# Optimization experiments

Measured on AMD Instinct MI355X. Metric: run time of the kernel, lower is better.

## Reference

```python
import jax, jax.numpy as jnp
import numpy as np

N_LAYERS = 3
NUM_USERS = 100000
NUM_ITEMS = 50000
N_NODES = NUM_USERS + NUM_ITEMS
N_EDGES = 6000000
EMB = 64


def setup_inputs() -> dict:
    key = jax.random.key(0)
    k1, k2, k3, k4, k5, k6, k7 = jax.random.split(key, 7)
    user_indices = jax.random.randint(k1, (1024,), 0, NUM_USERS)
    item_indices = jax.random.randint(k2, (1024,), 0, NUM_ITEMS)
    adj_src = jax.random.randint(k3, (N_EDGES,), 0, N_NODES)
    adj_dst = jax.random.randint(k4, (N_EDGES,), 0, N_NODES)
    # normalized adjacency values (stand-in for D^-1/2 A D^-1/2 entries)
    adj_vals = jax.random.uniform(k5, (N_EDGES,), dtype=jnp.float32) * 0.05
    user_emb = jax.random.normal(k6, (NUM_USERS, EMB), dtype=jnp.float32) * 0.1
    item_emb = jax.random.normal(k7, (NUM_ITEMS, EMB), dtype=jnp.float32) * 0.1
    return {
        "user_indices": user_indices,
        "item_indices": item_indices,
        "adj_src": adj_src,
        "adj_dst": adj_dst,
        "adj_vals": adj_vals,
        "user_emb": user_emb,
        "item_emb": item_emb,
    }


def reference(user_indices, item_indices, adj_src, adj_dst, adj_vals, user_emb, item_emb):
    # LightGCN.computer(): all_emb = cat(users, items); repeated SpMM; mean over layers
    all_emb = jnp.concatenate([user_emb, item_emb], axis=0)  # [N, d]
    n = all_emb.shape[0]
    cur = all_emb
    acc = all_emb  # running sum over layer embeddings (fused, avoids stacking)
    for _ in range(N_LAYERS):
        # SpMM in COO form: out[dst] += val * cur[src]
        msgs = adj_vals[:, None] * cur[adj_src]  # [E, d]
        cur = jax.ops.segment_sum(msgs, adj_dst, num_segments=n)
        acc = acc + cur
    light_out = acc / jnp.float32(N_LAYERS + 1)  # mean over (n_layers+1) embeddings
    # forward() returns cat(all_users, all_items) == light_out
    return light_out
```

## Files before the change

kernel.cpp:

```cpp
#include <hip/hip_runtime.h>


#define NUM_USERS 100000
#define NUM_ITEMS 50000
#define N_NODES   150000
#define EMB       64
#define N_EDGES   6000000

#define ROWS_PER_B 256
#define NBUCKETS   586
#define NROWS_PAD  (NBUCKETS * ROWS_PER_B)
#define PART_BLOCKS 256
#define CHUNK ((N_EDGES + PART_BLOCKS - 1) / PART_BLOCKS)

constexpr int NODE_F4 = N_NODES * EMB / 4;
constexpr int USER_F4 = NUM_USERS * EMB / 4;

typedef float f4v __attribute__((ext_vector_type(4)));

__device__ __forceinline__ float bf2f(unsigned short u) {
    union { unsigned int i; float f; } x; x.i = ((unsigned int)u) << 16; return x.f;
}
__device__ __forceinline__ unsigned short f2bf(float f) {
    union { float f; unsigned int i; } x; x.f = f;
    unsigned int b = x.i;
    return (unsigned short)((b + 0x7FFFu + ((b >> 16) & 1u)) >> 16);
}


__global__ void k_zero(int* __restrict__ p, int n) {
    int i = blockIdx.x * blockDim.x + threadIdx.x;
    if (i < n) p[i] = 0;
}

__global__ __launch_bounds__(256) void k_bhist(const int* __restrict__ dst,
                                               int* __restrict__ gcnt) {
    __shared__ int cnt[NBUCKETS];
    int t = threadIdx.x;
    for (int i = t; i < NBUCKETS; i += 256) cnt[i] = 0;
    __syncthreads();
    int e0 = blockIdx.x * CHUNK;
    int e1 = min(e0 + CHUNK, N_EDGES);
    int e = e0 + t;
    for (; e + 256 < e1; e += 512) {
        int b0 = __builtin_nontemporal_load(dst + e) >> 8;
        int b1 = __builtin_nontemporal_load(dst + e + 256) >> 8;
        atomicAdd(&cnt[b0], 1);
        atomicAdd(&cnt[b1], 1);
    }
    if (e < e1) atomicAdd(&cnt[__builtin_nontemporal_load(dst + e) >> 8], 1);
    __syncthreads();
    for (int i = t; i < NBUCKETS; i += 256)
        if (cnt[i]) atomicAdd(&gcnt[i], cnt[i]);
}

__global__ void k_bscan(const int* __restrict__ gcnt, int* __restrict__ boff,
                        int* __restrict__ gcur) {
    __shared__ int s[1024];
    int t = threadIdx.x;
    int x = (t < NBUCKETS) ? gcnt[t] : 0;
    s[t] = x;
    __syncthreads();
    for (int off = 1; off < 1024; off <<= 1) {
        int v = (t >= off) ? s[t - off] : 0;
        __syncthreads();
        s[t] += v;
        __syncthreads();
    }
    if (t < NBUCKETS) { int ex = s[t] - x; boff[t] = ex; gcur[t] = ex; }
    if (t == 0) boff[NBUCKETS] = N_EDGES;
}


__global__ __launch_bounds__(256) void k_part(const int* __restrict__ src,
                                              const int* __restrict__ dst,
                                              const float* __restrict__ val,
                                              int* __restrict__ gcur,
                                              int2* __restrict__ pairs) {
    __shared__ int cnt[NBUCKETS];
    __shared__ int base[NBUCKETS];
    int t = threadIdx.x;
    for (int i = t; i < NBUCKETS; i += 256) cnt[i] = 0;
    __syncthreads();
    int e0 = blockIdx.x * CHUNK;
    int e1 = min(e0 + CHUNK, N_EDGES);
    {
        int e = e0 + t;
        for (; e + 256 < e1; e += 512) {
            int b0 = __builtin_nontemporal_load(dst + e) >> 8;
            int b1 = __builtin_nontemporal_load(dst + e + 256) >> 8;
            atomicAdd(&cnt[b0], 1);
            atomicAdd(&cnt[b1], 1);
        }
        if (e < e1) atomicAdd(&cnt[__builtin_nontemporal_load(dst + e) >> 8], 1);
    }
    __syncthreads();
    for (int i = t; i < NBUCKETS; i += 256) {
        int c = cnt[i];
        base[i] = c ? atomicAdd(&gcur[i], c) : 0;
        cnt[i] = 0;
    }
    __syncthreads();
    {
        int e = e0 + t;
        for (; e + 256 < e1; e += 512) {
            int d0 = __builtin_nontemporal_load(dst + e);
            int s0 = __builtin_nontemporal_load(src + e);
            float v0 = __builtin_nontemporal_load(val + e);
            int d1 = __builtin_nontemporal_load(dst + e + 256);
            int s1 = __builtin_nontemporal_load(src + e + 256);
            float v1 = __builtin_nontemporal_load(val + e + 256);
            int b0 = d0 >> 8, b1 = d1 >> 8;
            int o0 = atomicAdd(&cnt[b0], 1);
            int o1 = atomicAdd(&cnt[b1], 1);
            pairs[base[b0] + o0] = make_int2(s0 | ((d0 & 255) << 18), __float_as_int(v0));
            pairs[base[b1] + o1] = make_int2(s1 | ((d1 & 255) << 18), __float_as_int(v1));
        }
        if (e < e1) {
            int d0 = __builtin_nontemporal_load(dst + e);
            int s0 = __builtin_nontemporal_load(src + e);
            float v0 = __builtin_nontemporal_load(val + e);
            int o0 = atomicAdd(&cnt[d0 >> 8], 1);
            pairs[base[d0 >> 8] + o0] = make_int2(s0 | ((d0 & 255) << 18),
                                                  __float_as_int(v0));
        }
    }
}


__global__ __launch_bounds__(256) void k_sort(const int* __restrict__ boff,
                                              const int2* __restrict__ pairs1,
                                              int2* __restrict__ pairs2,
                                              int* __restrict__ row_ptr) {
    __shared__ int cnt[ROWS_PER_B];
    __shared__ int s[ROWS_PER_B];
    int b = blockIdx.x;
    int t = threadIdx.x;
    cnt[t] = 0;
    __syncthreads();
    int beg = boff[b], end = boff[b + 1];
    {
        int e = beg + t;
        for (; e + 256 < end; e += 512) {
            int r0 = ((unsigned)pairs1[e].x) >> 18;
            int r1 = ((unsigned)pairs1[e + 256].x) >> 18;
            atomicAdd(&cnt[r0], 1);
            atomicAdd(&cnt[r1], 1);
        }
        if (e < end) atomicAdd(&cnt[((unsigned)pairs1[e].x) >> 18], 1);
    }
    __syncthreads();
    int x = cnt[t];
    s[t] = x;
    __syncthreads();
    for (int off = 1; off < 256; off <<= 1) {
        int v = (t >= off) ? s[t - off] : 0;
        __syncthreads();
        s[t] += v;
        __syncthreads();
    }
    int ex = beg + s[t] - x;
    row_ptr[b * ROWS_PER_B + t] = ex;
    if (b == NBUCKETS - 1 && t == 255) row_ptr[NROWS_PAD] = N_EDGES;
    __syncthreads();
    cnt[t] = ex;
    __syncthreads();
    const long* p1l = (const long*)pairs1;
    {
        int e = beg + t;
        for (; e + 256 < end; e += 512) {
            long q0 = __builtin_nontemporal_load(p1l + e);
            long q1 = __builtin_nontemporal_load(p1l + e + 256);
            int x0 = (int)q0, y0 = (int)(q0 >> 32);
            int x1 = (int)q1, y1 = (int)(q1 >> 32);
            int pos0 = atomicAdd(&cnt[((unsigned)x0) >> 18], 1);
            int pos1 = atomicAdd(&cnt[((unsigned)x1) >> 18], 1);
            pairs2[pos0] = make_int2(x0 & 0x3FFFF, y0);
            pairs2[pos1] = make_int2(x1 & 0x3FFFF, y1);
        }
        if (e < end) {
            long q0 = __builtin_nontemporal_load(p1l + e);
            int x0 = (int)q0, y0 = (int)(q0 >> 32);
            int pos0 = atomicAdd(&cnt[((unsigned)x0) >> 18], 1);
            pairs2[pos0] = make_int2(x0 & 0x3FFFF, y0);
        }
    }
}


__global__ void k_init(const f4v* __restrict__ ue, const f4v* __restrict__ ie,
                       ushort4* __restrict__ e0b, f4v* __restrict__ acc) {
    int i = blockIdx.x * blockDim.x + threadIdx.x;
    if (i >= NODE_F4) return;
    f4v v = (i < USER_F4) ? __builtin_nontemporal_load(ue + i)
                          : __builtin_nontemporal_load(ie + i - USER_F4);
    __builtin_nontemporal_store(v, acc + i);
    e0b[i] = make_ushort4(f2bf(v.x), f2bf(v.y), f2bf(v.z), f2bf(v.w));
}

__global__ __launch_bounds__(256) void k_spmm(const int* __restrict__ row_ptr,
                                              const long* __restrict__ pairs,
                                              const ushort4* __restrict__ cur,
                                              ushort4* __restrict__ nxt) {
    int tid = blockIdx.x * blockDim.x + threadIdx.x;
    int row = tid >> 4;
    if (row >= N_NODES) return;
    int c = tid & 15;
    int beg = row_ptr[row];
    int end = row_ptr[row + 1];
    float4 r = make_float4(0.f, 0.f, 0.f, 0.f);
    int k = beg;
    for (; k + 7 < end; k += 8) {
        long p[8];
        ushort4 g[8];
#pragma unroll
        for (int j = 0; j < 8; ++j) p[j] = pairs[k + j];
#pragma unroll
        for (int j = 0; j < 8; ++j) g[j] = cur[(long)(int)(p[j] & 0x3FFFF) * 16 + c];
#pragma unroll
        for (int j = 0; j < 8; ++j) {
            float v = __int_as_float((int)(p[j] >> 32));
            r.x += v * bf2f(g[j].x);
            r.y += v * bf2f(g[j].y);
            r.z += v * bf2f(g[j].z);
            r.w += v * bf2f(g[j].w);
        }
    }
    for (; k < end; ++k) {
        long p0 = pairs[k];
        ushort4 g0 = cur[(long)(int)(p0 & 0x3FFFF) * 16 + c];
        float v0 = __int_as_float((int)(p0 >> 32));
        r.x += v0 * bf2f(g0.x);
        r.y += v0 * bf2f(g0.y);
        r.z += v0 * bf2f(g0.z);
        r.w += v0 * bf2f(g0.w);
    }
    nxt[(long)row * 16 + c] = make_ushort4(f2bf(r.x), f2bf(r.y), f2bf(r.z), f2bf(r.w));
}

__global__ __launch_bounds__(256) void k_spmm_fin(const int* __restrict__ row_ptr,
                                                  const long* __restrict__ pairs,
                                                  const ushort4* __restrict__ cur,
                                                  const ushort4* __restrict__ e1b,
                                                  float4* __restrict__ acc) {
    int tid = blockIdx.x * blockDim.x + threadIdx.x;
    int row = tid >> 4;
    if (row >= N_NODES) return;
    int c = tid & 15;
    int beg = row_ptr[row];
    int end = row_ptr[row + 1];
    float4 r = make_float4(0.f, 0.f, 0.f, 0.f);
    int k = beg;
    for (; k + 7 < end; k += 8) {
        long p[8];
        ushort4 g[8];
#pragma unroll
        for (int j = 0; j < 8; ++j) p[j] = pairs[k + j];
#pragma unroll
        for (int j = 0; j < 8; ++j) g[j] = cur[(long)(int)(p[j] & 0x3FFFF) * 16 + c];
#pragma unroll
        for (int j = 0; j < 8; ++j) {
            float v = __int_as_float((int)(p[j] >> 32));
            r.x += v * bf2f(g[j].x);
            r.y += v * bf2f(g[j].y);
            r.z += v * bf2f(g[j].z);
            r.w += v * bf2f(g[j].w);
        }
    }
    for (; k < end; ++k) {
        long p0 = pairs[k];
        ushort4 g0 = cur[(long)(int)(p0 & 0x3FFFF) * 16 + c];
        float v0 = __int_as_float((int)(p0 >> 32));
        r.x += v0 * bf2f(g0.x);
        r.y += v0 * bf2f(g0.y);
        r.z += v0 * bf2f(g0.z);
        r.w += v0 * bf2f(g0.w);
    }
    long o = (long)row * 16 + c;
    ushort4 e1 = e1b[o];
    ushort4 e2 = cur[o];
    float4 a = acc[o];
    a.x = (a.x + bf2f(e1.x) + bf2f(e2.x) + r.x) * 0.25f;
    a.y = (a.y + bf2f(e1.y) + bf2f(e2.y) + r.y) * 0.25f;
    a.z = (a.z + bf2f(e1.z) + bf2f(e2.z) + r.z) * 0.25f;
    a.w = (a.w + bf2f(e1.w) + bf2f(e2.w) + r.w) * 0.25f;
    acc[o] = a;
}


__global__ void lgcn_init(const float4* __restrict__ user_emb,
                          const float4* __restrict__ item_emb,
                          float4* __restrict__ cur, float4* __restrict__ nxt,
                          float4* __restrict__ acc) {
    int i = blockIdx.x * blockDim.x + threadIdx.x;
    if (i >= NODE_F4) return;
    float4 v = (i < USER_F4) ? user_emb[i] : item_emb[i - USER_F4];
    cur[i] = v; acc[i] = v; nxt[i] = make_float4(0.f, 0.f, 0.f, 0.f);
}

__global__ void lgcn_scatter(const int* __restrict__ src, const int* __restrict__ dst,
                             const float* __restrict__ val,
                             const float4* __restrict__ cur, float* __restrict__ nxt) {
    int tid = blockIdx.x * blockDim.x + threadIdx.x;
    int e = tid >> 4;
    if (e >= N_EDGES) return;
    int c = tid & 15;
    int s = src[e]; int d = dst[e]; float v = val[e];
    float4 m = cur[(long)s * 16 + c];
    float* p = nxt + (long)d * 64 + c * 4;
    unsafeAtomicAdd(p + 0, v * m.x);
    unsafeAtomicAdd(p + 1, v * m.y);
    unsafeAtomicAdd(p + 2, v * m.z);
    unsafeAtomicAdd(p + 3, v * m.w);
}

__global__ void lgcn_add_zero(float4* __restrict__ acc, const float4* __restrict__ nxt,
                              float4* __restrict__ other) {
    int i = blockIdx.x * blockDim.x + threadIdx.x;
    if (i >= NODE_F4) return;
    float4 a = acc[i]; float4 n = nxt[i];
    a.x += n.x; a.y += n.y; a.z += n.z; a.w += n.w;
    acc[i] = a;
    other[i] = make_float4(0.f, 0.f, 0.f, 0.f);
}

__global__ void lgcn_final(float4* __restrict__ acc, const float4* __restrict__ nxt) {
    int i = blockIdx.x * blockDim.x + threadIdx.x;
    if (i >= NODE_F4) return;
    float4 a = acc[i]; float4 n = nxt[i];
    a.x = (a.x + n.x) * 0.25f; a.y = (a.y + n.y) * 0.25f;
    a.z = (a.z + n.z) * 0.25f; a.w = (a.w + n.w) * 0.25f;
    acc[i] = a;
}


extern "C" void kernel_launch(void* const* d_in, const int* in_sizes, int n_in,
                              void* d_out, int out_size, void* d_ws, size_t ws_size,
                              hipStream_t stream) {
    const int*    adj_src  = (const int*)d_in[2];
    const int*    adj_dst  = (const int*)d_in[3];
    const float*  adj_vals = (const float*)d_in[4];
    float* acc = (float*)d_out;

    const int BLK = 256;
    const int grid_node  = (NODE_F4 + BLK - 1) / BLK;
    const int grid_row16 = (N_NODES * 16 + BLK - 1) / BLK;

    const size_t SZ_PAIRS = (size_t)N_EDGES * 8;
    const size_t SZ_BF    = (size_t)N_NODES * EMB * 2;
    const size_t SZ_RP    = 600320;
    const size_t SZ_B     = 4096;
    const size_t NEEDED   = 2 * SZ_PAIRS + SZ_BF + SZ_RP + 3 * SZ_B;

    if (ws_size >= NEEDED) {
        char* w = (char*)d_ws;
        int2*    pairs2 = (int2*)(w);
        int2*    pairs1 = (int2*)(w + SZ_PAIRS);
        ushort4* e0b    = (ushort4*)(w + SZ_PAIRS);
        ushort4* e1b    = (ushort4*)(w + SZ_PAIRS + SZ_BF);
        ushort4* e2b    = (ushort4*)(w + 2 * SZ_PAIRS);
        int*  row_ptr= (int*)(w + 2 * SZ_PAIRS + SZ_BF);
        int*  gcnt   = (int*)(w + 2 * SZ_PAIRS + SZ_BF + SZ_RP);
        int*  boff   = (int*)(w + 2 * SZ_PAIRS + SZ_BF + SZ_RP + SZ_B);
        int*  gcur   = (int*)(w + 2 * SZ_PAIRS + SZ_BF + SZ_RP + 2 * SZ_B);

        k_zero<<<(NBUCKETS + BLK - 1) / BLK, BLK, 0, stream>>>(gcnt, NBUCKETS);
        k_bhist<<<PART_BLOCKS, BLK, 0, stream>>>(adj_dst, gcnt);
        k_bscan<<<1, 1024, 0, stream>>>(gcnt, boff, gcur);

        k_part<<<PART_BLOCKS, BLK, 0, stream>>>(adj_src, adj_dst, adj_vals, gcur, pairs1);

        k_sort<<<NBUCKETS, BLK, 0, stream>>>(boff, pairs1, pairs2, row_ptr);

        k_init<<<grid_node, BLK, 0, stream>>>((const f4v*)d_in[5], (const f4v*)d_in[6],
                                              e0b, (f4v*)acc);
        k_spmm<<<grid_row16, BLK, 0, stream>>>(row_ptr, (const long*)pairs2, e0b, e1b);
        k_spmm<<<grid_row16, BLK, 0, stream>>>(row_ptr, (const long*)pairs2, e1b, e2b);
        k_spmm_fin<<<grid_row16, BLK, 0, stream>>>(row_ptr, (const long*)pairs2, e2b,
                                                   e1b, (float4*)acc);
    } else {
        const float4* user_emb = (const float4*)d_in[5];
        const float4* item_emb = (const float4*)d_in[6];
        float* ws0 = (float*)d_ws;
        float* ws1 = ws0 + (size_t)N_NODES * EMB;
        lgcn_init<<<grid_node, BLK, 0, stream>>>(user_emb, item_emb,
                                                 (float4*)ws0, (float4*)ws1, (float4*)acc);
        lgcn_scatter<<<(N_EDGES*16+BLK-1)/BLK, BLK, 0, stream>>>(adj_src, adj_dst, adj_vals,
                                                    (const float4*)ws0, ws1);
        lgcn_add_zero<<<grid_node, BLK, 0, stream>>>((float4*)acc, (const float4*)ws1, (float4*)ws0);
        lgcn_scatter<<<(N_EDGES*16+BLK-1)/BLK, BLK, 0, stream>>>(adj_src, adj_dst, adj_vals,
                                                    (const float4*)ws1, ws0);
        lgcn_add_zero<<<grid_node, BLK, 0, stream>>>((float4*)acc, (const float4*)ws0, (float4*)ws1);
        lgcn_scatter<<<(N_EDGES*16+BLK-1)/BLK, BLK, 0, stream>>>(adj_src, adj_dst, adj_vals,
                                                    (const float4*)ws0, ws1);
        lgcn_final<<<grid_node, BLK, 0, stream>>>((float4*)acc, (const float4*)ws1);
    }
}
```

Baseline: 663.7 us.

## Replace two-pass bucket partition sort with direct per-row histogram and atomic placement

The CSR build no longer partitions edges into 256-row buckets and then sorts within each bucket. It now builds a per-destination-row histogram with global atomics, scans it hierarchically, and scatters each edge straight to its final slot through per-row atomic cursors. This drops one full pass over the pairs array and the intermediate buffer. In exchange it relies on heavy global atomic traffic and uncoalesced 8-byte scatters, and edge order within a row becomes nondeterministic.

```diff
diff --git a/kernel.cpp b/kernel.cpp
--- a/kernel.cpp
+++ b/kernel.cpp
@@ -10,8 +10,9 @@
 #define ROWS_PER_B 256
 #define NBUCKETS   586
 #define NROWS_PAD  (NBUCKETS * ROWS_PER_B)
-#define PART_BLOCKS 256
-#define CHUNK ((N_EDGES + PART_BLOCKS - 1) / PART_BLOCKS)
+
+#define HIST_BLOCKS  2048
+#define PLACE_BLOCKS 2048
 
 constexpr int NODE_F4 = N_NODES * EMB / 4;
 constexpr int USER_F4 = NUM_USERS * EMB / 4;
@@ -33,29 +34,28 @@
     if (i < n) p[i] = 0;
 }
 
-__global__ __launch_bounds__(256) void k_bhist(const int* __restrict__ dst,
-                                               int* __restrict__ gcnt) {
-    __shared__ int cnt[NBUCKETS];
-    int t = threadIdx.x;
-    for (int i = t; i < NBUCKETS; i += 256) cnt[i] = 0;
+__global__ __launch_bounds__(256) void k_rhist(const int* __restrict__ dst,
+                                               int* __restrict__ rcnt) {
+    int e = blockIdx.x * 256 + threadIdx.x;
+    int stride = gridDim.x * 256;
+    for (; e < N_EDGES; e += stride)
+        atomicAdd(&rcnt[dst[e]], 1);
+}
+
+__global__ __launch_bounds__(256) void k_bsum(const int* __restrict__ rcnt,
+                                              int* __restrict__ gcnt) {
+    __shared__ int s[256];
+    int b = blockIdx.x, t = threadIdx.x;
+    s[t] = rcnt[b * 256 + t];
     __syncthreads();
-    int e0 = blockIdx.x * CHUNK;
-    int e1 = min(e0 + CHUNK, N_EDGES);
-    int e = e0 + t;
-    for (; e + 256 < e1; e += 512) {
-        int b0 = __builtin_nontemporal_load(dst + e) >> 8;
-        int b1 = __builtin_nontemporal_load(dst + e + 256) >> 8;
-        atomicAdd(&cnt[b0], 1);
-        atomicAdd(&cnt[b1], 1);
-    }
-    if (e < e1) atomicAdd(&cnt[__builtin_nontemporal_load(dst + e) >> 8], 1);
-    __syncthreads();
-    for (int i = t; i < NBUCKETS; i += 256)
-        if (cnt[i]) atomicAdd(&gcnt[i], cnt[i]);
-}
-
-__global__ void k_bscan(const int* __restrict__ gcnt, int* __restrict__ boff,
-                        int* __restrict__ gcur) {
+    for (int off = 128; off > 0; off >>= 1) {
+        if (t < off) s[t] += s[t + off];
+        __syncthreads();
+    }
+    if (t == 0) gcnt[b] = s[0];
+}
+
+__global__ void k_bscan(const int* __restrict__ gcnt, int* __restrict__ boff) {
     __shared__ int s[1024];
     int t = threadIdx.x;
     int x = (t < NBUCKETS) ? gcnt[t] : 0;
@@ -67,90 +67,17 @@
         s[t] += v;
         __syncthreads();
     }
-    if (t < NBUCKETS) { int ex = s[t] - x; boff[t] = ex; gcur[t] = ex; }
+    if (t < NBUCKETS) boff[t] = s[t] - x;
     if (t == 0) boff[NBUCKETS] = N_EDGES;
 }
 
-
-__global__ __launch_bounds__(256) void k_part(const int* __restrict__ src,
-                                              const int* __restrict__ dst,
-                                              const float* __restrict__ val,
-                                              int* __restrict__ gcur,
-                                              int2* __restrict__ pairs) {
-    __shared__ int cnt[NBUCKETS];
-    __shared__ int base[NBUCKETS];
-    int t = threadIdx.x;
-    for (int i = t; i < NBUCKETS; i += 256) cnt[i] = 0;
-    __syncthreads();
-    int e0 = blockIdx.x * CHUNK;
-    int e1 = min(e0 + CHUNK, N_EDGES);
-    {
-        int e = e0 + t;
-        for (; e + 256 < e1; e += 512) {
-            int b0 = __builtin_nontemporal_load(dst + e) >> 8;
-            int b1 = __builtin_nontemporal_load(dst + e + 256) >> 8;
-            atomicAdd(&cnt[b0], 1);
-            atomicAdd(&cnt[b1], 1);
-        }
-        if (e < e1) atomicAdd(&cnt[__builtin_nontemporal_load(dst + e) >> 8], 1);
-    }
-    __syncthreads();
-    for (int i = t; i < NBUCKETS; i += 256) {
-        int c = cnt[i];
-        base[i] = c ? atomicAdd(&gcur[i], c) : 0;
-        cnt[i] = 0;
-    }
-    __syncthreads();
-    {
-        int e = e0 + t;
-        for (; e + 256 < e1; e += 512) {
-            int d0 = __builtin_nontemporal_load(dst + e);
-            int s0 = __builtin_nontemporal_load(src + e);
-            float v0 = __builtin_nontemporal_load(val + e);
-            int d1 = __builtin_nontemporal_load(dst + e + 256);
-            int s1 = __builtin_nontemporal_load(src + e + 256);
-            float v1 = __builtin_nontemporal_load(val + e + 256);
-            int b0 = d0 >> 8, b1 = d1 >> 8;
-            int o0 = atomicAdd(&cnt[b0], 1);
-            int o1 = atomicAdd(&cnt[b1], 1);
-            pairs[base[b0] + o0] = make_int2(s0 | ((d0 & 255) << 18), __float_as_int(v0));
-            pairs[base[b1] + o1] = make_int2(s1 | ((d1 & 255) << 18), __float_as_int(v1));
-        }
-        if (e < e1) {
-            int d0 = __builtin_nontemporal_load(dst + e);
-            int s0 = __builtin_nontemporal_load(src + e);
-            float v0 = __builtin_nontemporal_load(val + e);
-            int o0 = atomicAdd(&cnt[d0 >> 8], 1);
-            pairs[base[d0 >> 8] + o0] = make_int2(s0 | ((d0 & 255) << 18),
-                                                  __float_as_int(v0));
-        }
-    }
-}
-
-
-__global__ __launch_bounds__(256) void k_sort(const int* __restrict__ boff,
-                                              const int2* __restrict__ pairs1,
-                                              int2* __restrict__ pairs2,
-                                              int* __restrict__ row_ptr) {
-    __shared__ int cnt[ROWS_PER_B];
-    __shared__ int s[ROWS_PER_B];
-    int b = blockIdx.x;
-    int t = threadIdx.x;
-    cnt[t] = 0;
-    __syncthreads();
-    int beg = boff[b], end = boff[b + 1];
-    {
-        int e = beg + t;
-        for (; e + 256 < end; e += 512) {
-            int r0 = ((unsigned)pairs1[e].x) >> 18;
-            int r1 = ((unsigned)pairs1[e + 256].x) >> 18;
-            atomicAdd(&cnt[r0], 1);
-            atomicAdd(&cnt[r1], 1);
-        }
-        if (e < end) atomicAdd(&cnt[((unsigned)pairs1[e].x) >> 18], 1);
-    }
-    __syncthreads();
-    int x = cnt[t];
+__global__ __launch_bounds__(256) void k_rscan(const int* __restrict__ rcnt,
+                                               const int* __restrict__ boff,
+                                               int* __restrict__ row_ptr,
+                                               int* __restrict__ gcur) {
+    __shared__ int s[256];
+    int b = blockIdx.x, t = threadIdx.x;
+    int x = rcnt[b * 256 + t];
     s[t] = x;
     __syncthreads();
     for (int off = 1; off < 256; off <<= 1) {
@@ -159,31 +86,26 @@
         s[t] += v;
         __syncthreads();
     }
-    int ex = beg + s[t] - x;
-    row_ptr[b * ROWS_PER_B + t] = ex;
+    int ex = boff[b] + s[t] - x;
+    row_ptr[b * 256 + t] = ex;
+    gcur[b * 256 + t] = ex;
     if (b == NBUCKETS - 1 && t == 255) row_ptr[NROWS_PAD] = N_EDGES;
-    __syncthreads();
-    cnt[t] = ex;
-    __syncthreads();
-    const long* p1l = (const long*)pairs1;
-    {
-        int e = beg + t;
-        for (; e + 256 < end; e += 512) {
-            long q0 = __builtin_nontemporal_load(p1l + e);
-            long q1 = __builtin_nontemporal_load(p1l + e + 256);
-            int x0 = (int)q0, y0 = (int)(q0 >> 32);
-            int x1 = (int)q1, y1 = (int)(q1 >> 32);
-            int pos0 = atomicAdd(&cnt[((unsigned)x0) >> 18], 1);
-            int pos1 = atomicAdd(&cnt[((unsigned)x1) >> 18], 1);
-            pairs2[pos0] = make_int2(x0 & 0x3FFFF, y0);
-            pairs2[pos1] = make_int2(x1 & 0x3FFFF, y1);
-        }
-        if (e < end) {
-            long q0 = __builtin_nontemporal_load(p1l + e);
-            int x0 = (int)q0, y0 = (int)(q0 >> 32);
-            int pos0 = atomicAdd(&cnt[((unsigned)x0) >> 18], 1);
-            pairs2[pos0] = make_int2(x0 & 0x3FFFF, y0);
-        }
+}
+
+
+__global__ __launch_bounds__(256) void k_place(const int* __restrict__ src,
+                                               const int* __restrict__ dst,
+                                               const float* __restrict__ val,
+                                               int* __restrict__ gcur,
+                                               int2* __restrict__ pairs2) {
+    int e = blockIdx.x * 256 + threadIdx.x;
+    int stride = gridDim.x * 256;
+    for (; e < N_EDGES; e += stride) {
+        int d = dst[e];
+        int s = src[e];
+        float v = val[e];
+        int pos = atomicAdd(&gcur[d], 1);
+        pairs2[pos] = make_int2(s, __float_as_int(v));
     }
 }
 
@@ -349,28 +271,30 @@
     const size_t SZ_PAIRS = (size_t)N_EDGES * 8;
     const size_t SZ_BF    = (size_t)N_NODES * EMB * 2;
     const size_t SZ_RP    = 600320;
+    const size_t SZ_CNT   = 600320;
     const size_t SZ_B     = 4096;
-    const size_t NEEDED   = 2 * SZ_PAIRS + SZ_BF + SZ_RP + 3 * SZ_B;
+    const size_t NEEDED   = SZ_PAIRS + 3 * SZ_BF + SZ_RP + 2 * SZ_CNT + 2 * SZ_B;
 
     if (ws_size >= NEEDED) {
         char* w = (char*)d_ws;
         int2*    pairs2 = (int2*)(w);
-        int2*    pairs1 = (int2*)(w + SZ_PAIRS);
         ushort4* e0b    = (ushort4*)(w + SZ_PAIRS);
         ushort4* e1b    = (ushort4*)(w + SZ_PAIRS + SZ_BF);
-        ushort4* e2b    = (ushort4*)(w + 2 * SZ_PAIRS);
-        int*  row_ptr= (int*)(w + 2 * SZ_PAIRS + SZ_BF);
-        int*  gcnt   = (int*)(w + 2 * SZ_PAIRS + SZ_BF + SZ_RP);
-        int*  boff   = (int*)(w + 2 * SZ_PAIRS + SZ_BF + SZ_RP + SZ_B);
-        int*  gcur   = (int*)(w + 2 * SZ_PAIRS + SZ_BF + SZ_RP + 2 * SZ_B);
-
-        k_zero<<<(NBUCKETS + BLK - 1) / BLK, BLK, 0, stream>>>(gcnt, NBUCKETS);
-        k_bhist<<<PART_BLOCKS, BLK, 0, stream>>>(adj_dst, gcnt);
-        k_bscan<<<1, 1024, 0, stream>>>(gcnt, boff, gcur);
-
-        k_part<<<PART_BLOCKS, BLK, 0, stream>>>(adj_src, adj_dst, adj_vals, gcur, pairs1);
-
-        k_sort<<<NBUCKETS, BLK, 0, stream>>>(boff, pairs1, pairs2, row_ptr);
+        ushort4* e2b    = (ushort4*)(w + SZ_PAIRS + 2 * SZ_BF);
+        int* row_ptr = (int*)(w + SZ_PAIRS + 3 * SZ_BF);
+        int* rcnt    = (int*)(w + SZ_PAIRS + 3 * SZ_BF + SZ_RP);
+        int* gcur    = (int*)(w + SZ_PAIRS + 3 * SZ_BF + SZ_RP + SZ_CNT);
+        int* gcnt    = (int*)(w + SZ_PAIRS + 3 * SZ_BF + SZ_RP + 2 * SZ_CNT);
+        int* boff    = (int*)(w + SZ_PAIRS + 3 * SZ_BF + SZ_RP + 2 * SZ_CNT + SZ_B);
+
+        k_zero<<<(NROWS_PAD + BLK - 1) / BLK, BLK, 0, stream>>>(rcnt, NROWS_PAD);
+        k_rhist<<<HIST_BLOCKS, BLK, 0, stream>>>(adj_dst, rcnt);
+        k_bsum<<<NBUCKETS, BLK, 0, stream>>>(rcnt, gcnt);
+        k_bscan<<<1, 1024, 0, stream>>>(gcnt, boff);
+        k_rscan<<<NBUCKETS, BLK, 0, stream>>>(rcnt, boff, row_ptr, gcur);
+
+        k_place<<<PLACE_BLOCKS, BLK, 0, stream>>>(adj_src, adj_dst, adj_vals,
+                                                  gcur, pairs2);
 
         k_init<<<grid_node, BLK, 0, stream>>>((const f4v*)d_in[5], (const f4v*)d_in[6],
                                               e0b, (f4v*)acc);
```

Result: slower. 999.5 us (+50.6%).
